# Performance work log

Measured on AMD Instinct MI355X. Metric: run time of the kernel, lower is better.

The kernel has to match this reference:

```python
import jax, jax.numpy as jnp
import numpy as np

B, NV, NS, L = 32, 2048, 512, 64
FEAT, SEM, HID, ATT, DM = 1024, 512, 512, 512, 512


def setup_inputs() -> dict:
    key = jax.random.key(0)
    ks = jax.random.split(key, 14)
    s = lambda k, sh: jax.random.normal(k, sh, dtype=jnp.float32) * 0.02
    return {
        "query": jax.random.normal(ks[0], (B, 1, HID), dtype=jnp.float32),
        "visual_features": jax.random.normal(ks[1], (B, NV, FEAT), dtype=jnp.float32),
        "semantic_features": jax.random.normal(ks[2], (B, NS, SEM), dtype=jnp.float32),
        "patient_info": jax.random.normal(ks[3], (B, L, DM), dtype=jnp.float32),
        "W1v": s(ks[4], (HID, ATT)),
        "W2v": s(ks[5], (FEAT, ATT)),
        "vv": s(ks[6], (ATT, 1)),
        "W3": s(ks[7], (DM, ATT)),
        "b3": jnp.zeros((ATT,), dtype=jnp.float32),
        "W1s": s(ks[8], (HID, ATT)),
        "W2s": s(ks[9], (SEM, ATT)),
        "vs": s(ks[10], (ATT, 1)),
        "W": s(ks[11], (FEAT + SEM, FEAT)),
        "bW": jnp.zeros((FEAT,), dtype=jnp.float32),
    }


def reference(query, visual_features, semantic_features, patient_info,
              W1v, W2v, vv, W3, b3, W1s, W2s, vs, W, bW):
    # mean over patient sequence, project: [B,1,ATT]
    pinfo = jnp.mean(patient_info, axis=1, keepdims=True) @ W3 + b3
    q_v = query @ W1v          # [B,1,ATT]
    # visual branch
    v_scores = jnp.tanh(q_v + visual_features @ W2v + pinfo) @ vv  # [B,NV,1]
    v_attn = jax.nn.softmax(v_scores, axis=1)
    # semantic branch
    q_s = query @ W1s
    s_scores = jnp.tanh(q_s + semantic_features @ W2s + pinfo) @ vs  # [B,NS,1]
    s_attn = jax.nn.softmax(s_scores, axis=1)
    ctx = jnp.concatenate([
        jnp.sum(visual_features * v_attn, axis=1),    # [B,FEAT]
        jnp.sum(semantic_features * s_attn, axis=1),  # [B,SEM]
    ], axis=1) @ W + bW
    return ctx, v_attn, s_attn
```

## Files before the change

kernel.cpp:

```cpp
#include <hip/hip_runtime.h>

typedef float f32x4 __attribute__((ext_vector_type(4)));
typedef short short8 __attribute__((ext_vector_type(8)));

#define B_    32
#define NV_   2048
#define NS_   512
#define L_    64
#define FEAT_ 1024
#define SEM_  512
#define HID_  512
#define ATT_  512
#define DM_   512

#define FENCE asm volatile("" ::: "memory")

__device__ __forceinline__ unsigned int f2bf_pk(float lo, float hi) {
  unsigned int ul = (__float_as_uint(lo) + 0x8000u) >> 16;
  unsigned int uh = (__float_as_uint(hi) + 0x8000u) & 0xffff0000u;
  return uh | ul;
}

__device__ __forceinline__ unsigned short f2bf(float f) {
  return (unsigned short)((__float_as_uint(f) + 0x8000u) >> 16);
}

__device__ __forceinline__ float bflo(unsigned int u) { return __uint_as_float(u << 16); }
__device__ __forceinline__ float bfhi(unsigned int u) { return __uint_as_float(u & 0xffff0000u); }

__device__ __forceinline__ float fast_tanh(float x) {
  float e = __expf(2.f * x);
  return 1.f - 2.f * __builtin_amdgcn_rcpf(e + 1.f);
}

__device__ __forceinline__ void gload16(const void* g, void* l) {
  __builtin_amdgcn_global_load_lds(
      (const __attribute__((address_space(1))) unsigned char*)g,
      (__attribute__((address_space(3))) unsigned char*)l, 16, 0, 0);
}

__global__ __launch_bounds__(256) void k_pmean(const float* __restrict__ pat,
                                               float* __restrict__ pm) {
  int b = blockIdx.x, t = threadIdx.x;
  for (int d = t; d < DM_; d += 256) {
    float s = 0.f;
    for (int l = 0; l < L_; ++l) s += pat[(b * L_ + l) * DM_ + d];
    pm[b * DM_ + d] = s * (1.f / 64.f);
  }
}

__global__ __launch_bounds__(256) void k_qp(const float* __restrict__ query,
                                            const float* __restrict__ pm,
                                            const float* __restrict__ W1v,
                                            const float* __restrict__ W1s,
                                            const float* __restrict__ W3,
                                            const float* __restrict__ b3,
                                            float* __restrict__ qpv,
                                            float* __restrict__ qps) {
  int idx = blockIdx.x * 256 + threadIdx.x;
  int b = idx >> 9, a = idx & 511;
  float pi = b3[a];
  for (int d = 0; d < DM_; ++d) pi += pm[b * DM_ + d] * W3[d * ATT_ + a];
  float qv = 0.f, qs = 0.f;
  for (int h = 0; h < HID_; ++h) {
    float q = query[b * HID_ + h];
    qv += q * W1v[h * ATT_ + a];
    qs += q * W1s[h * ATT_ + a];
  }
  qpv[idx] = qv + pi;
  qps[idx] = qs + pi;
}

__global__ __launch_bounds__(256) void k_swz(const float* __restrict__ W2,
                                             unsigned short* __restrict__ out,
                                             int total) {
  int idx = blockIdx.x * 256 + threadIdx.x;
  if (idx >= total) return;
  int k = idx >> 9, c = idx & 511;
  int kc = k >> 5, kr = k & 31, q = kr >> 3, j = kr & 7;
  int cb = c >> 4, n = c & 15;
  out[(kc * 32 + cb) * 512 + q * 128 + n * 8 + j] = f2bf(W2[idx]);
}

__global__ __launch_bounds__(256, 2) void k_scores_fused(
    const float* __restrict__ X, const unsigned short* __restrict__ Wt,
    const float* __restrict__ qp, const float* __restrict__ vvec,
    float* __restrict__ score, unsigned short* __restrict__ Av,
    int K, int rows_per_batch) {
  __shared__ __align__(16) float AsF[3 * 2048];
  const int t = threadIdx.x;
  const int lane = t & 63, wave = t >> 6;
  const int quad = lane >> 4, l15 = lane & 15;
  const int row0 = blockIdx.x * 64;
  const int b = row0 / rows_per_batch;
  const int nk = K >> 5;
  const int rt128 = blockIdx.x >> 1;
  const int rbOff = (blockIdx.x & 1) * 4;

  const int g_hi = lane >> 3, g_lo = lane & 7;
  const int sub = g_lo ^ (g_hi & 7);
  const int kofs = (sub >> 1) * 8 + (sub & 1) * 4;
  const float* gsrc0 = X + (size_t)(row0 + wave * 16 + g_hi) * K + kofs;
  const float* gsrc1 = X + (size_t)(row0 + wave * 16 + 8 + g_hi) * K + kofs;

  const int swz = (l15 & 7) << 4;
  const int ro0 = (l15 * 128 + quad * 32) ^ swz;
  const int ro1 = (l15 * 128 + quad * 32 + 16) ^ swz;

  char* avB = (char*)(Av + (size_t)rt128 * nk * 4096) + rbOff * 1024 + quad * 256 + l15 * 16;
  const char* gB = (const char*)Wt + (size_t)wave * 8192 + lane * 16;

  const f32x4 zero = {0.f, 0.f, 0.f, 0.f};
  f32x4 acc[4][8];
#pragma unroll
  for (int a = 0; a < 4; ++a)
#pragma unroll
    for (int cb = 0; cb < 8; ++cb) acc[a][cb] = zero;

  {
    char* d0 = (char*)AsF + wave * 2048;
    gload16(gsrc0, d0);
    gload16(gsrc1, d0 + 1024);
    char* d1 = (char*)AsF + 8192 + wave * 2048;
    gload16(gsrc0 + 32, d1);
    gload16(gsrc1 + 32, d1 + 1024);
  }
  asm volatile("s_waitcnt vmcnt(2)" ::: "memory");

  for (int kc = 0; kc < nk; ++kc) {
    short8 bfr[8];
    const char* gBk = gB + (size_t)kc * 32768;
#pragma unroll
    for (int cb = 0; cb < 8; ++cb)
      bfr[cb] = *(const short8*)(gBk + cb * 1024);

    FENCE;
    __builtin_amdgcn_s_barrier();
    FENCE;

    const char* bufR = (const char*)AsF + (kc % 3) * 8192;
    uint4 u[4];
#pragma unroll
    for (int a = 0; a < 4; ++a) {
      f32x4 lo = *(const f32x4*)(bufR + a * 2048 + ro0);
      f32x4 hi = *(const f32x4*)(bufR + a * 2048 + ro1);
      uint4 v;
      v.x = f2bf_pk(lo.x, lo.y);
      v.y = f2bf_pk(lo.z, lo.w);
      v.z = f2bf_pk(hi.x, hi.y);
      v.w = f2bf_pk(hi.z, hi.w);
      u[a] = v;
    }
    if (wave == 0) {
      char* avK = avB + (size_t)kc * 8192;
#pragma unroll
      for (int a = 0; a < 4; ++a) *(uint4*)(avK + a * 1024) = u[a];
    }
#pragma unroll
    for (int a = 0; a < 4; ++a) {
      short8 af = (short8&)u[a];
#pragma unroll
      for (int cb = 0; cb < 8; ++cb)
        acc[a][cb] = __builtin_amdgcn_mfma_f32_16x16x32_bf16(af, bfr[cb], acc[a][cb], 0, 0, 0);
    }

    if (kc + 2 < nk) {
      char* d = (char*)AsF + ((kc + 2) % 3) * 8192 + wave * 2048;
      gload16(gsrc0 + (size_t)(kc + 2) * 32, d);
      gload16(gsrc1 + (size_t)(kc + 2) * 32, d + 1024);
    }
  }

  float qv_[8], vw_[8];
#pragma unroll
  for (int cb = 0; cb < 8; ++cb) {
    int col = wave * 128 + cb * 16 + l15;
    qv_[cb] = qp[b * ATT_ + col];
    vw_[cb] = vvec[col];
  }
#pragma unroll
  for (int a = 0; a < 4; ++a) {
#pragma unroll
    for (int rr = 0; rr < 4; ++rr) {
      float s = 0.f;
#pragma unroll
      for (int cb = 0; cb < 8; ++cb)
        s += fast_tanh(acc[a][cb][rr] + qv_[cb]) * vw_[cb];
      s += __shfl_xor(s, 1);
      s += __shfl_xor(s, 2);
      s += __shfl_xor(s, 4);
      s += __shfl_xor(s, 8);
      if (l15 == 0) atomicAdd(&score[row0 + a * 16 + quad * 4 + rr], s);
    }
  }
}

__global__ __launch_bounds__(256) void k_scores_f32(const float* __restrict__ X,
                                                    const unsigned short* __restrict__ Wt,
                                                    const float* __restrict__ qp,
                                                    const float* __restrict__ vvec,
                                                    float* __restrict__ score,
                                                    int K, int rows_per_batch) {
  __shared__ __align__(16) unsigned short As[4096];
  __shared__ __align__(16) unsigned short Bs[4096];
  const int t = threadIdx.x;
  const int lane = t & 63;
  const int wave = t >> 6;
  const int wr = wave & 1, wc = wave >> 1;
  const int quad = lane >> 4, l15 = lane & 15;
  const int row0 = blockIdx.x * 128;
  const int ct = blockIdx.y;
  const int b = row0 / rows_per_batch;

  const int ai_row = t >> 3;
  const int ai_k0 = (t & 7) * 4;
  const int a_q = ai_k0 >> 3;
  const int a_j0 = ai_k0 & 7;

  const f32x4 zero = {0.f, 0.f, 0.f, 0.f};
  f32x4 acc[4][4];
#pragma unroll
  for (int a = 0; a < 4; ++a)
#pragma unroll
    for (int bb = 0; bb < 4; ++bb) acc[a][bb] = zero;

  const int nk = K >> 5;
  for (int kc = 0; kc < nk; ++kc) {
    __syncthreads();
#pragma unroll
    for (int ii = 0; ii < 4; ++ii) {
      int i = ii * 32 + ai_row;
      const float4 v = *(const float4*)(X + (size_t)(row0 + i) * K + kc * 32 + ai_k0);
      uint2 h;
      h.x = f2bf_pk(v.x, v.y);
      h.y = f2bf_pk(v.z, v.w);
      int rb = i >> 4, m = i & 15;
      *(uint2*)(As + rb * 512 + a_q * 128 + m * 8 + a_j0) = h;
    }
    {
      const uint4* src = (const uint4*)(Wt + (size_t)(kc * 32 + ct * 8) * 512);
      uint4* dst = (uint4*)Bs;
      dst[t] = src[t];
      dst[t + 256] = src[t + 256];
    }
    __syncthreads();
    short8 af[4], bfr[4];
#pragma unroll
    for (int a = 0; a < 4; ++a)
      af[a] = *(const short8*)(As + (wr * 4 + a) * 512 + quad * 128 + l15 * 8);
#pragma unroll
    for (int bb = 0; bb < 4; ++bb)
      bfr[bb] = *(const short8*)(Bs + (wc * 4 + bb) * 512 + quad * 128 + l15 * 8);
#pragma unroll
    for (int a = 0; a < 4; ++a)
#pragma unroll
      for (int bb = 0; bb < 4; ++bb)
        acc[a][bb] = __builtin_amdgcn_mfma_f32_16x16x32_bf16(af[a], bfr[bb], acc[a][bb], 0, 0, 0);
  }

  const int colbase = ct * 128 + wc * 64;
  float qv_[4], vw_[4];
#pragma unroll
  for (int bb = 0; bb < 4; ++bb) {
    int col = colbase + bb * 16 + l15;
    qv_[bb] = qp[b * ATT_ + col];
    vw_[bb] = vvec[col];
  }
#pragma unroll
  for (int a = 0; a < 4; ++a) {
#pragma unroll
    for (int r = 0; r < 4; ++r) {
      float s = 0.f;
#pragma unroll
      for (int bb = 0; bb < 4; ++bb)
        s += fast_tanh(acc[a][bb][r] + qv_[bb]) * vw_[bb];
      s += __shfl_xor(s, 1);
      s += __shfl_xor(s, 2);
      s += __shfl_xor(s, 4);
      s += __shfl_xor(s, 8);
      if (l15 == 0) {
        int row = row0 + wr * 64 + a * 16 + quad * 4 + r;
        atomicAdd(&score[row], s);
      }
    }
  }
}

__global__ __launch_bounds__(256) void k_softmax(const float* __restrict__ score,
                                                 float* __restrict__ attn, int N) {
  __shared__ float sm[4];
  int b = blockIdx.x, t = threadIdx.x;
  const float* s = score + (size_t)b * N;
  float m = -1e30f;
  for (int i = t; i < N; i += 256) m = fmaxf(m, s[i]);
  for (int k = 32; k; k >>= 1) m = fmaxf(m, __shfl_xor(m, k));
  if ((t & 63) == 0) sm[t >> 6] = m;
  __syncthreads();
  m = fmaxf(fmaxf(sm[0], sm[1]), fmaxf(sm[2], sm[3]));
  __syncthreads();
  float sum = 0.f;
  for (int i = t; i < N; i += 256) sum += __expf(s[i] - m);
  for (int k = 32; k; k >>= 1) sum += __shfl_xor(sum, k);
  if ((t & 63) == 0) sm[t >> 6] = sum;
  __syncthreads();
  sum = sm[0] + sm[1] + sm[2] + sm[3];
  float inv = 1.f / sum;
  for (int i = t; i < N; i += 256) attn[(size_t)b * N + i] = __expf(s[i] - m) * inv;
}

__global__ __launch_bounds__(256) void k_wsum_swz(const unsigned short* __restrict__ Aswz,
                                                  const float* __restrict__ attn,
                                                  float* __restrict__ ctx_pre,
                                                  int nkc, int rtPerBatch,
                                                  int rowsPerBatch, int colOff) {
  const int b = blockIdx.x, kc = blockIdx.y;
  const int t = threadIdx.x, q = t >> 6, l = t & 63;
  const int rbl = l >> 4, m = l & 15;
  float acc[8] = {0.f, 0.f, 0.f, 0.f, 0.f, 0.f, 0.f, 0.f};
  for (int rt = 0; rt < rtPerBatch; ++rt) {
    const unsigned short* blk = Aswz + ((size_t)(b * rtPerBatch + rt) * nkc + kc) * 4096;
    const float* ab = attn + (size_t)b * rowsPerBatch + rt * 128;
#pragma unroll
    for (int p = 0; p < 2; ++p) {
      int rb = p * 4 + rbl;
      float a = ab[rb * 16 + m];
      uint4 v = *(const uint4*)(blk + rb * 512 + q * 128 + m * 8);
      acc[0] += a * bflo(v.x);
      acc[1] += a * bfhi(v.x);
      acc[2] += a * bflo(v.y);
      acc[3] += a * bfhi(v.y);
      acc[4] += a * bflo(v.z);
      acc[5] += a * bfhi(v.z);
      acc[6] += a * bflo(v.w);
      acc[7] += a * bfhi(v.w);
    }
  }
#pragma unroll
  for (int off = 1; off < 64; off <<= 1) {
#pragma unroll
    for (int j = 0; j < 8; ++j) acc[j] += __shfl_xor(acc[j], off);
  }
  if (l == 0) {
    float* dst = ctx_pre + b * 1536 + colOff + kc * 32 + q * 8;
#pragma unroll
    for (int j = 0; j < 8; ++j) dst[j] = acc[j];
  }
}

__global__ __launch_bounds__(256) void k_wsum(const float* __restrict__ feats,
                                              const float* __restrict__ attn,
                                              float* __restrict__ ctx_pre,
                                              int N, int F, int colOff, int rowsPerChunk) {
  int b = blockIdx.x, rc = blockIdx.y, t = threadIdx.x;
  int c4 = t * 4;
  if (c4 >= F) return;
  int r0 = rc * rowsPerChunk;
  const float* fb = feats + ((size_t)b * N + r0) * F;
  const float* ab = attn + (size_t)b * N + r0;
  float4 acc = {0.f, 0.f, 0.f, 0.f};
  for (int r = 0; r < rowsPerChunk; ++r) {
    float a = ab[r];
    float4 v = *(const float4*)(fb + (size_t)r * F + c4);
    acc.x += a * v.x; acc.y += a * v.y; acc.z += a * v.z; acc.w += a * v.w;
  }
  float* dst = ctx_pre + b * 1536 + colOff + c4;
  atomicAdd(dst + 0, acc.x);
  atomicAdd(dst + 1, acc.y);
  atomicAdd(dst + 2, acc.z);
  atomicAdd(dst + 3, acc.w);
}

__global__ __launch_bounds__(256) void k_final(const float* __restrict__ cp,
                                               const float* __restrict__ W,
                                               const float* __restrict__ bW,
                                               float* __restrict__ out) {
  int b = blockIdx.x, oc = blockIdx.y, t = threadIdx.x;
  int o = oc * 256 + t;
  float acc = bW[o];
  const float* c = cp + b * 1536;
  for (int k = 0; k < 1536; ++k) acc += c[k] * W[k * FEAT_ + o];
  out[b * FEAT_ + o] = acc;
}

extern "C" void kernel_launch(void* const* d_in, const int* in_sizes, int n_in,
                              void* d_out, int out_size, void* d_ws, size_t ws_size,
                              hipStream_t stream) {
  const float* query = (const float*)d_in[0];
  const float* vf    = (const float*)d_in[1];
  const float* sf    = (const float*)d_in[2];
  const float* pat   = (const float*)d_in[3];
  const float* W1v   = (const float*)d_in[4];
  const float* W2v   = (const float*)d_in[5];
  const float* vv    = (const float*)d_in[6];
  const float* W3    = (const float*)d_in[7];
  const float* b3    = (const float*)d_in[8];
  const float* W1s   = (const float*)d_in[9];
  const float* W2s   = (const float*)d_in[10];
  const float* vs    = (const float*)d_in[11];
  const float* W     = (const float*)d_in[12];
  const float* bW    = (const float*)d_in[13];
  float* out = (float*)d_out;

  char* ws = (char*)d_ws;
  float* scores_v = (float*)(ws);
  float* scores_s = (float*)(ws + 262144);
  float* ctx_pre  = (float*)(ws + 327680);
  float* pm   = (float*)(ws + 524288);
  float* qpv  = (float*)(ws + 589824);
  float* qps  = (float*)(ws + 655360);
  unsigned short* Wtv = (unsigned short*)(ws + 720896);
  unsigned short* Wts = (unsigned short*)(ws + 720896 + 1048576);
  unsigned short* Av  = (unsigned short*)(ws + 4194304);
  unsigned short* Asm = (unsigned short*)(ws + 4194304 + 134217728);
  const size_t NEED = 4194304ull + 134217728ull + 16777216ull;
  const bool bf16path = (ws_size >= NEED);

  hipMemsetAsync(d_ws, 0, bf16path ? 327680 : 524288, stream);

  k_pmean<<<32, 256, 0, stream>>>(pat, pm);
  k_qp<<<64, 256, 0, stream>>>(query, pm, W1v, W1s, W3, b3, qpv, qps);
  k_swz<<<(FEAT_ * ATT_) / 256, 256, 0, stream>>>(W2v, Wtv, FEAT_ * ATT_);
  k_swz<<<(SEM_ * ATT_) / 256, 256, 0, stream>>>(W2s, Wts, SEM_ * ATT_);

  float* v_attn = out + B_ * FEAT_;
  float* s_attn = out + B_ * FEAT_ + B_ * NV_;

  if (bf16path) {
    k_scores_fused<<<(B_ * NV_) / 64, 256, 0, stream>>>(vf, Wtv, qpv, vv, scores_v, Av, FEAT_, NV_);
    k_scores_fused<<<(B_ * NS_) / 64, 256, 0, stream>>>(sf, Wts, qps, vs, scores_s, Asm, SEM_, NS_);
    k_softmax<<<B_, 256, 0, stream>>>(scores_v, v_attn, NV_);
    k_softmax<<<B_, 256, 0, stream>>>(scores_s, s_attn, NS_);
    k_wsum_swz<<<dim3(B_, FEAT_ / 32), 256, 0, stream>>>(Av, v_attn, ctx_pre, FEAT_ / 32, NV_ / 128, NV_, 0);
    k_wsum_swz<<<dim3(B_, SEM_ / 32), 256, 0, stream>>>(Asm, s_attn, ctx_pre, SEM_ / 32, NS_ / 128, NS_, 1024);
  } else {
    k_scores_f32<<<dim3((B_ * NV_) / 128, 4), 256, 0, stream>>>(vf, Wtv, qpv, vv, scores_v, FEAT_, NV_);
    k_scores_f32<<<dim3((B_ * NS_) / 128, 4), 256, 0, stream>>>(sf, Wts, qps, vs, scores_s, SEM_, NS_);
    k_softmax<<<B_, 256, 0, stream>>>(scores_v, v_attn, NV_);
    k_softmax<<<B_, 256, 0, stream>>>(scores_s, s_attn, NS_);
    k_wsum<<<dim3(B_, 8), 256, 0, stream>>>(vf, v_attn, ctx_pre, NV_, FEAT_, 0, 256);
    k_wsum<<<dim3(B_, 2), 256, 0, stream>>>(sf, s_attn, ctx_pre, NS_, SEM_, 1024, 256);
  }

  k_final<<<dim3(B_, 4), 256, 0, stream>>>(ctx_pre, W, bW, out);
}
```

Baseline: 686.5 us.

## Drop bf16 activation side-buffer, deepen LDS prefetch, merge small kernels

The scores kernel no longer writes a bf16 copy of the features for later reuse. The weighted sum now re-reads the original fp32 features directly, which removes about 150 MB of extra writes but makes the wsum pass read fp32 data. The A-tile prefetch ring grows from 3 to 5 LDS buffers, and loads are issued right after the barrier. The pmean, swizzle, softmax and wsum launches are merged into combined kernels to cut launch count.

```diff
diff --git a/kernel.cpp b/kernel.cpp
--- a/kernel.cpp
+++ b/kernel.cpp
@@ -25,9 +25,6 @@
   return (unsigned short)((__float_as_uint(f) + 0x8000u) >> 16);
 }
 
-__device__ __forceinline__ float bflo(unsigned int u) { return __uint_as_float(u << 16); }
-__device__ __forceinline__ float bfhi(unsigned int u) { return __uint_as_float(u & 0xffff0000u); }
-
 __device__ __forceinline__ float fast_tanh(float x) {
   float e = __expf(2.f * x);
   return 1.f - 2.f * __builtin_amdgcn_rcpf(e + 1.f);
@@ -39,63 +36,67 @@
       (__attribute__((address_space(3))) unsigned char*)l, 16, 0, 0);
 }
 
-__global__ __launch_bounds__(256) void k_pmean(const float* __restrict__ pat,
-                                               float* __restrict__ pm) {
-  int b = blockIdx.x, t = threadIdx.x;
-  for (int d = t; d < DM_; d += 256) {
-    float s = 0.f;
-    for (int l = 0; l < L_; ++l) s += pat[(b * L_ + l) * DM_ + d];
-    pm[b * DM_ + d] = s * (1.f / 64.f);
-  }
-}
-
 __global__ __launch_bounds__(256) void k_qp(const float* __restrict__ query,
-                                            const float* __restrict__ pm,
+                                            const float* __restrict__ pat,
                                             const float* __restrict__ W1v,
                                             const float* __restrict__ W1s,
                                             const float* __restrict__ W3,
                                             const float* __restrict__ b3,
                                             float* __restrict__ qpv,
                                             float* __restrict__ qps) {
-  int idx = blockIdx.x * 256 + threadIdx.x;
-  int b = idx >> 9, a = idx & 511;
+  __shared__ float pmL[DM_];
+  const int t = threadIdx.x;
+  const int b = blockIdx.x >> 1;
+  for (int d = t; d < DM_; d += 256) {
+    float s = 0.f;
+    for (int l = 0; l < L_; ++l) s += pat[(b * L_ + l) * DM_ + d];
+    pmL[d] = s * (1.f / 64.f);
+  }
+  __syncthreads();
+  const int a = (blockIdx.x & 1) * 256 + t;
   float pi = b3[a];
-  for (int d = 0; d < DM_; ++d) pi += pm[b * DM_ + d] * W3[d * ATT_ + a];
+  for (int d = 0; d < DM_; ++d) pi += pmL[d] * W3[d * ATT_ + a];
   float qv = 0.f, qs = 0.f;
   for (int h = 0; h < HID_; ++h) {
     float q = query[b * HID_ + h];
     qv += q * W1v[h * ATT_ + a];
     qs += q * W1s[h * ATT_ + a];
   }
-  qpv[idx] = qv + pi;
-  qps[idx] = qs + pi;
-}
-
-__global__ __launch_bounds__(256) void k_swz(const float* __restrict__ W2,
-                                             unsigned short* __restrict__ out,
-                                             int total) {
+  qpv[b * ATT_ + a] = qv + pi;
+  qps[b * ATT_ + a] = qs + pi;
+}
+
+__global__ __launch_bounds__(256) void k_swz2(const float* __restrict__ W2v,
+                                              const float* __restrict__ W2s,
+                                              unsigned short* __restrict__ outV,
+                                              unsigned short* __restrict__ outS) {
   int idx = blockIdx.x * 256 + threadIdx.x;
-  if (idx >= total) return;
+  const float* src;
+  unsigned short* dst;
+  if (idx < FEAT_ * ATT_) {
+    src = W2v; dst = outV;
+  } else {
+    idx -= FEAT_ * ATT_;
+    if (idx >= SEM_ * ATT_) return;
+    src = W2s; dst = outS;
+  }
   int k = idx >> 9, c = idx & 511;
   int kc = k >> 5, kr = k & 31, q = kr >> 3, j = kr & 7;
   int cb = c >> 4, n = c & 15;
-  out[(kc * 32 + cb) * 512 + q * 128 + n * 8 + j] = f2bf(W2[idx]);
+  dst[(kc * 32 + cb) * 512 + q * 128 + n * 8 + j] = f2bf(src[idx]);
 }
 
 __global__ __launch_bounds__(256, 2) void k_scores_fused(
     const float* __restrict__ X, const unsigned short* __restrict__ Wt,
     const float* __restrict__ qp, const float* __restrict__ vvec,
-    float* __restrict__ score, unsigned short* __restrict__ Av,
-    int K, int rows_per_batch) {
-  __shared__ __align__(16) float AsF[3 * 2048];
+    float* __restrict__ score, int K, int rows_per_batch) {
+  __shared__ __align__(16) float AsF[5 * 2048];
   const int t = threadIdx.x;
   const int lane = t & 63, wave = t >> 6;
   const int quad = lane >> 4, l15 = lane & 15;
   const int row0 = blockIdx.x * 64;
   const int b = row0 / rows_per_batch;
   const int nk = K >> 5;
-  const int rt128 = blockIdx.x >> 1;
-  const int rbOff = (blockIdx.x & 1) * 4;
 
   const int g_hi = lane >> 3, g_lo = lane & 7;
   const int sub = g_lo ^ (g_hi & 7);
@@ -107,7 +108,6 @@
   const int ro0 = (l15 * 128 + quad * 32) ^ swz;
   const int ro1 = (l15 * 128 + quad * 32 + 16) ^ swz;
 
-  char* avB = (char*)(Av + (size_t)rt128 * nk * 4096) + rbOff * 1024 + quad * 256 + l15 * 16;
   const char* gB = (const char*)Wt + (size_t)wave * 8192 + lane * 16;
 
   const f32x4 zero = {0.f, 0.f, 0.f, 0.f};
@@ -117,15 +117,13 @@
 #pragma unroll
     for (int cb = 0; cb < 8; ++cb) acc[a][cb] = zero;
 
-  {
-    char* d0 = (char*)AsF + wave * 2048;
-    gload16(gsrc0, d0);
-    gload16(gsrc1, d0 + 1024);
-    char* d1 = (char*)AsF + 8192 + wave * 2048;
-    gload16(gsrc0 + 32, d1);
-    gload16(gsrc1 + 32, d1 + 1024);
-  }
-  asm volatile("s_waitcnt vmcnt(2)" ::: "memory");
+#pragma unroll
+  for (int p = 0; p < 4; ++p) {
+    char* d = (char*)AsF + p * 8192 + wave * 2048;
+    gload16(gsrc0 + (size_t)p * 32, d);
+    gload16(gsrc1 + (size_t)p * 32, d + 1024);
+  }
+  asm volatile("s_waitcnt vmcnt(6)" ::: "memory");
 
   for (int kc = 0; kc < nk; ++kc) {
     short8 bfr[8];
@@ -138,8 +136,15 @@
     __builtin_amdgcn_s_barrier();
     FENCE;
 
-    const char* bufR = (const char*)AsF + (kc % 3) * 8192;
-    uint4 u[4];
+    {
+      const int kn = (kc + 4 < nk) ? kc + 4 : nk - 1;
+      char* d = (char*)AsF + ((kc + 4) % 5) * 8192 + wave * 2048;
+      gload16(gsrc0 + (size_t)kn * 32, d);
+      gload16(gsrc1 + (size_t)kn * 32, d + 1024);
+    }
+    FENCE;
+
+    const char* bufR = (const char*)AsF + (kc % 5) * 8192;
 #pragma unroll
     for (int a = 0; a < 4; ++a) {
       f32x4 lo = *(const f32x4*)(bufR + a * 2048 + ro0);
@@ -149,25 +154,10 @@
       v.y = f2bf_pk(lo.z, lo.w);
       v.z = f2bf_pk(hi.x, hi.y);
       v.w = f2bf_pk(hi.z, hi.w);
-      u[a] = v;
-    }
-    if (wave == 0) {
-      char* avK = avB + (size_t)kc * 8192;
-#pragma unroll
-      for (int a = 0; a < 4; ++a) *(uint4*)(avK + a * 1024) = u[a];
-    }
-#pragma unroll
-    for (int a = 0; a < 4; ++a) {
-      short8 af = (short8&)u[a];
+      short8 af = (short8&)v;
 #pragma unroll
       for (int cb = 0; cb < 8; ++cb)
         acc[a][cb] = __builtin_amdgcn_mfma_f32_16x16x32_bf16(af, bfr[cb], acc[a][cb], 0, 0, 0);
-    }
-
-    if (kc + 2 < nk) {
-      char* d = (char*)AsF + ((kc + 2) % 3) * 8192 + wave * 2048;
-      gload16(gsrc0 + (size_t)(kc + 2) * 32, d);
-      gload16(gsrc1 + (size_t)(kc + 2) * 32, d + 1024);
     }
   }
 
@@ -195,102 +185,17 @@
   }
 }
 
-__global__ __launch_bounds__(256) void k_scores_f32(const float* __restrict__ X,
-                                                    const unsigned short* __restrict__ Wt,
-                                                    const float* __restrict__ qp,
-                                                    const float* __restrict__ vvec,
-                                                    float* __restrict__ score,
-                                                    int K, int rows_per_batch) {
-  __shared__ __align__(16) unsigned short As[4096];
-  __shared__ __align__(16) unsigned short Bs[4096];
-  const int t = threadIdx.x;
-  const int lane = t & 63;
-  const int wave = t >> 6;
-  const int wr = wave & 1, wc = wave >> 1;
-  const int quad = lane >> 4, l15 = lane & 15;
-  const int row0 = blockIdx.x * 128;
-  const int ct = blockIdx.y;
-  const int b = row0 / rows_per_batch;
-
-  const int ai_row = t >> 3;
-  const int ai_k0 = (t & 7) * 4;
-  const int a_q = ai_k0 >> 3;
-  const int a_j0 = ai_k0 & 7;
-
-  const f32x4 zero = {0.f, 0.f, 0.f, 0.f};
-  f32x4 acc[4][4];
-#pragma unroll
-  for (int a = 0; a < 4; ++a)
-#pragma unroll
-    for (int bb = 0; bb < 4; ++bb) acc[a][bb] = zero;
-
-  const int nk = K >> 5;
-  for (int kc = 0; kc < nk; ++kc) {
-    __syncthreads();
-#pragma unroll
-    for (int ii = 0; ii < 4; ++ii) {
-      int i = ii * 32 + ai_row;
-      const float4 v = *(const float4*)(X + (size_t)(row0 + i) * K + kc * 32 + ai_k0);
-      uint2 h;
-      h.x = f2bf_pk(v.x, v.y);
-      h.y = f2bf_pk(v.z, v.w);
-      int rb = i >> 4, m = i & 15;
-      *(uint2*)(As + rb * 512 + a_q * 128 + m * 8 + a_j0) = h;
-    }
-    {
-      const uint4* src = (const uint4*)(Wt + (size_t)(kc * 32 + ct * 8) * 512);
-      uint4* dst = (uint4*)Bs;
-      dst[t] = src[t];
-      dst[t + 256] = src[t + 256];
-    }
-    __syncthreads();
-    short8 af[4], bfr[4];
-#pragma unroll
-    for (int a = 0; a < 4; ++a)
-      af[a] = *(const short8*)(As + (wr * 4 + a) * 512 + quad * 128 + l15 * 8);
-#pragma unroll
-    for (int bb = 0; bb < 4; ++bb)
-      bfr[bb] = *(const short8*)(Bs + (wc * 4 + bb) * 512 + quad * 128 + l15 * 8);
-#pragma unroll
-    for (int a = 0; a < 4; ++a)
-#pragma unroll
-      for (int bb = 0; bb < 4; ++bb)
-        acc[a][bb] = __builtin_amdgcn_mfma_f32_16x16x32_bf16(af[a], bfr[bb], acc[a][bb], 0, 0, 0);
-  }
-
-  const int colbase = ct * 128 + wc * 64;
-  float qv_[4], vw_[4];
-#pragma unroll
-  for (int bb = 0; bb < 4; ++bb) {
-    int col = colbase + bb * 16 + l15;
-    qv_[bb] = qp[b * ATT_ + col];
-    vw_[bb] = vvec[col];
-  }
-#pragma unroll
-  for (int a = 0; a < 4; ++a) {
-#pragma unroll
-    for (int r = 0; r < 4; ++r) {
-      float s = 0.f;
-#pragma unroll
-      for (int bb = 0; bb < 4; ++bb)
-        s += fast_tanh(acc[a][bb][r] + qv_[bb]) * vw_[bb];
-      s += __shfl_xor(s, 1);
-      s += __shfl_xor(s, 2);
-      s += __shfl_xor(s, 4);
-      s += __shfl_xor(s, 8);
-      if (l15 == 0) {
-        int row = row0 + wr * 64 + a * 16 + quad * 4 + r;
-        atomicAdd(&score[row], s);
-      }
-    }
-  }
-}
-
-__global__ __launch_bounds__(256) void k_softmax(const float* __restrict__ score,
-                                                 float* __restrict__ attn, int N) {
+__global__ __launch_bounds__(256) void k_softmax2(const float* __restrict__ scores_v,
+                                                  const float* __restrict__ scores_s,
+                                                  float* __restrict__ v_attn,
+                                                  float* __restrict__ s_attn) {
   __shared__ float sm[4];
-  int b = blockIdx.x, t = threadIdx.x;
-  const float* s = score + (size_t)b * N;
+  const int bb = blockIdx.x, t = threadIdx.x;
+  const float* s;
+  float* dst;
+  int N;
+  if (bb < 32) { s = scores_v + (size_t)bb * NV_; dst = v_attn + (size_t)bb * NV_; N = NV_; }
+  else         { s = scores_s + (size_t)(bb - 32) * NS_; dst = s_attn + (size_t)(bb - 32) * NS_; N = NS_; }
   float m = -1e30f;
   for (int i = t; i < N; i += 256) m = fmaxf(m, s[i]);
   for (int k = 32; k; k >>= 1) m = fmaxf(m, __shfl_xor(m, k));
@@ -305,60 +210,27 @@
   __syncthreads();
   sum = sm[0] + sm[1] + sm[2] + sm[3];
   float inv = 1.f / sum;
-  for (int i = t; i < N; i += 256) attn[(size_t)b * N + i] = __expf(s[i] - m) * inv;
-}
-
-__global__ __launch_bounds__(256) void k_wsum_swz(const unsigned short* __restrict__ Aswz,
-                                                  const float* __restrict__ attn,
-                                                  float* __restrict__ ctx_pre,
-                                                  int nkc, int rtPerBatch,
-                                                  int rowsPerBatch, int colOff) {
-  const int b = blockIdx.x, kc = blockIdx.y;
-  const int t = threadIdx.x, q = t >> 6, l = t & 63;
-  const int rbl = l >> 4, m = l & 15;
-  float acc[8] = {0.f, 0.f, 0.f, 0.f, 0.f, 0.f, 0.f, 0.f};
-  for (int rt = 0; rt < rtPerBatch; ++rt) {
-    const unsigned short* blk = Aswz + ((size_t)(b * rtPerBatch + rt) * nkc + kc) * 4096;
-    const float* ab = attn + (size_t)b * rowsPerBatch + rt * 128;
-#pragma unroll
-    for (int p = 0; p < 2; ++p) {
-      int rb = p * 4 + rbl;
-      float a = ab[rb * 16 + m];
-      uint4 v = *(const uint4*)(blk + rb * 512 + q * 128 + m * 8);
-      acc[0] += a * bflo(v.x);
-      acc[1] += a * bfhi(v.x);
-      acc[2] += a * bflo(v.y);
-      acc[3] += a * bfhi(v.y);
-      acc[4] += a * bflo(v.z);
-      acc[5] += a * bfhi(v.z);
-      acc[6] += a * bflo(v.w);
-      acc[7] += a * bfhi(v.w);
-    }
-  }
-#pragma unroll
-  for (int off = 1; off < 64; off <<= 1) {
-#pragma unroll
-    for (int j = 0; j < 8; ++j) acc[j] += __shfl_xor(acc[j], off);
-  }
-  if (l == 0) {
-    float* dst = ctx_pre + b * 1536 + colOff + kc * 32 + q * 8;
-#pragma unroll
-    for (int j = 0; j < 8; ++j) dst[j] = acc[j];
-  }
-}
-
-__global__ __launch_bounds__(256) void k_wsum(const float* __restrict__ feats,
-                                              const float* __restrict__ attn,
-                                              float* __restrict__ ctx_pre,
-                                              int N, int F, int colOff, int rowsPerChunk) {
-  int b = blockIdx.x, rc = blockIdx.y, t = threadIdx.x;
-  int c4 = t * 4;
+  for (int i = t; i < N; i += 256) dst[i] = __expf(s[i] - m) * inv;
+}
+
+__global__ __launch_bounds__(256) void k_wsum2(const float* __restrict__ vf,
+                                               const float* __restrict__ sf,
+                                               const float* __restrict__ v_attn,
+                                               const float* __restrict__ s_attn,
+                                               float* __restrict__ ctx_pre) {
+  const int b = blockIdx.x, y = blockIdx.y, t = threadIdx.x;
+  const float* feats;
+  const float* attn;
+  int N, F, colOff, r0;
+  if (y < 8) { feats = vf; attn = v_attn; N = NV_; F = FEAT_; colOff = 0;     r0 = y * 256; }
+  else       { feats = sf; attn = s_attn; N = NS_; F = SEM_;  colOff = 1024;  r0 = (y - 8) * 256; }
+  const int c4 = t * 4;
   if (c4 >= F) return;
-  int r0 = rc * rowsPerChunk;
   const float* fb = feats + ((size_t)b * N + r0) * F;
   const float* ab = attn + (size_t)b * N + r0;
   float4 acc = {0.f, 0.f, 0.f, 0.f};
-  for (int r = 0; r < rowsPerChunk; ++r) {
+#pragma unroll 4
+  for (int r = 0; r < 256; ++r) {
     float a = ab[r];
     float4 v = *(const float4*)(fb + (size_t)r * F + c4);
     acc.x += a * v.x; acc.y += a * v.y; acc.z += a * v.z; acc.w += a * v.w;
@@ -405,41 +277,22 @@
   float* scores_v = (float*)(ws);
   float* scores_s = (float*)(ws + 262144);
   float* ctx_pre  = (float*)(ws + 327680);
-  float* pm   = (float*)(ws + 524288);
-  float* qpv  = (float*)(ws + 589824);
-  float* qps  = (float*)(ws + 655360);
-  unsigned short* Wtv = (unsigned short*)(ws + 720896);
-  unsigned short* Wts = (unsigned short*)(ws + 720896 + 1048576);
-  unsigned short* Av  = (unsigned short*)(ws + 4194304);
-  unsigned short* Asm = (unsigned short*)(ws + 4194304 + 134217728);
-  const size_t NEED = 4194304ull + 134217728ull + 16777216ull;
-  const bool bf16path = (ws_size >= NEED);
-
-  hipMemsetAsync(d_ws, 0, bf16path ? 327680 : 524288, stream);
-
-  k_pmean<<<32, 256, 0, stream>>>(pat, pm);
-  k_qp<<<64, 256, 0, stream>>>(query, pm, W1v, W1s, W3, b3, qpv, qps);
-  k_swz<<<(FEAT_ * ATT_) / 256, 256, 0, stream>>>(W2v, Wtv, FEAT_ * ATT_);
-  k_swz<<<(SEM_ * ATT_) / 256, 256, 0, stream>>>(W2s, Wts, SEM_ * ATT_);
+  float* qpv      = (float*)(ws + 524288);
+  float* qps      = (float*)(ws + 589824);
+  unsigned short* Wtv = (unsigned short*)(ws + 655360);
+  unsigned short* Wts = (unsigned short*)(ws + 655360 + 1048576);
+
+  hipMemsetAsync(d_ws, 0, 524288, stream);
+
+  k_swz2<<<(FEAT_ * ATT_ + SEM_ * ATT_) / 256, 256, 0, stream>>>(W2v, W2s, Wtv, Wts);
+  k_qp<<<64, 256, 0, stream>>>(query, pat, W1v, W1s, W3, b3, qpv, qps);
 
   float* v_attn = out + B_ * FEAT_;
   float* s_attn = out + B_ * FEAT_ + B_ * NV_;
 
-  if (bf16path) {
-    k_scores_fused<<<(B_ * NV_) / 64, 256, 0, stream>>>(vf, Wtv, qpv, vv, scores_v, Av, FEAT_, NV_);
-    k_scores_fused<<<(B_ * NS_) / 64, 256, 0, stream>>>(sf, Wts, qps, vs, scores_s, Asm, SEM_, NS_);
-    k_softmax<<<B_, 256, 0, stream>>>(scores_v, v_attn, NV_);
-    k_softmax<<<B_, 256, 0, stream>>>(scores_s, s_attn, NS_);
-    k_wsum_swz<<<dim3(B_, FEAT_ / 32), 256, 0, stream>>>(Av, v_attn, ctx_pre, FEAT_ / 32, NV_ / 128, NV_, 0);
-    k_wsum_swz<<<dim3(B_, SEM_ / 32), 256, 0, stream>>>(Asm, s_attn, ctx_pre, SEM_ / 32, NS_ / 128, NS_, 1024);
-  } else {
-    k_scores_f32<<<dim3((B_ * NV_) / 128, 4), 256, 0, stream>>>(vf, Wtv, qpv, vv, scores_v, FEAT_, NV_);
-    k_scores_f32<<<dim3((B_ * NS_) / 128, 4), 256, 0, stream>>>(sf, Wts, qps, vs, scores_s, SEM_, NS_);
-    k_softmax<<<B_, 256, 0, stream>>>(scores_v, v_attn, NV_);
-    k_softmax<<<B_, 256, 0, stream>>>(scores_s, s_attn, NS_);
-    k_wsum<<<dim3(B_, 8), 256, 0, stream>>>(vf, v_attn, ctx_pre, NV_, FEAT_, 0, 256);
-    k_wsum<<<dim3(B_, 2), 256, 0, stream>>>(sf, s_attn, ctx_pre, NS_, SEM_, 1024, 256);
-  }
-
+  k_scores_fused<<<(B_ * NV_) / 64, 256, 0, stream>>>(vf, Wtv, qpv, vv, scores_v, FEAT_, NV_);
+  k_scores_fused<<<(B_ * NS_) / 64, 256, 0, stream>>>(sf, Wts, qps, vs, scores_s, SEM_, NS_);
+  k_softmax2<<<64, 256, 0, stream>>>(scores_v, scores_s, v_attn, s_attn);
+  k_wsum2<<<dim3(B_, 10), 256, 0, stream>>>(vf, sf, v_attn, s_attn, ctx_pre);
   k_final<<<dim3(B_, 4), 256, 0, stream>>>(ctx_pre, W, bW, out);
 }
```

New measurement: 659.1 us. 4.0% less time.
